# Performance work log

Hardware: AMD Instinct MI355X
Metric: run time of the kernel (lower is better)

The kernel has to match this reference:

```python
import jax, jax.numpy as jnp
import numpy as np

COMMITMENT_COST = 0.25

def setup_inputs() -> dict:
    key = jax.random.key(0)
    k1, k2 = jax.random.split(key)
    inputs = jax.random.normal(k1, (16, 256, 64, 64), dtype=jnp.float32)   # [B, C=D, H, W]
    embedding = jax.random.normal(k2, (2048, 256), dtype=jnp.float32)      # [K, D] codebook
    return {"inputs": inputs, "embedding": embedding}

def reference(inputs, embedding):
    K, D = embedding.shape
    x = jnp.transpose(inputs, (0, 2, 3, 1))            # [B, H, W, D]
    flat = x.reshape(-1, D)                            # [N, D]
    distances = (jnp.sum(flat * flat, axis=1, keepdims=True)
                 + jnp.sum(embedding * embedding, axis=1)
                 - 2.0 * flat @ embedding.T)
    idx = jnp.argmin(distances, axis=1)                # [N]
    encodings = jax.nn.one_hot(idx, K, dtype=flat.dtype)  # [N, K]
    quantized = embedding[idx].reshape(x.shape)        # gather == one_hot @ embedding
    # commitment loss (eval mode: only e_latent term, scaled)
    e_latent_loss = jnp.mean((jax.lax.stop_gradient(quantized) - x) ** 2)
    loss = COMMITMENT_COST * e_latent_loss
    # straight-through estimator
    quantized_st = x + jax.lax.stop_gradient(quantized - x)
    avg_probs = jnp.mean(encodings, axis=0)
    perplexity = jnp.exp(-jnp.sum(avg_probs * jnp.log(avg_probs + 1e-10)))
    return (loss,
            jnp.transpose(quantized_st, (0, 3, 1, 2)),  # back to [B, C, H, W]
            perplexity,
            encodings)
```

## Files before the change

### kernel.cpp

```cpp
#include <hip/hip_runtime.h>

#define KCODES  2048
#define DDIM    256

#define OUT_LOSS 0
#define OUT_Q    1
#define OUT_PERP 16777217
#define OUT_ENC  16777218

#define WS_IDX  0
#define WS_E2   1048576
#define WS_CNT  1056768
#define WS_SUM  1064960
#define WS_EHI  2097152

typedef _Float16 f16x8 __attribute__((ext_vector_type(8)));
typedef _Float16 f16x4 __attribute__((ext_vector_type(4)));
typedef float    f32x4 __attribute__((ext_vector_type(4)));
typedef float    f32x2 __attribute__((ext_vector_type(2)));

#define MERGE2(m1,i1,m2,i2,n1,j1,n2,j2)                                   \
    {                                                                     \
        const bool w_ = ((n1) < (m1)) || ((n1) == (m1) && (j1) < (i1));   \
        const float w1_ = w_ ? (n1) : (m1); const int wi_ = w_ ? (j1) : (i1); \
        const float l1_ = w_ ? (m1) : (n1); const int li_ = w_ ? (i1) : (j1); \
        const float c2_ = w_ ? (n2) : (m2); const int ci_ = w_ ? (j2) : (i2); \
        const bool s_ = ((c2_) < (l1_)) || ((c2_) == (l1_) && (ci_) < (li_)); \
        (m1) = w1_; (i1) = wi_;                                           \
        (m2) = s_ ? c2_ : l1_; (i2) = s_ ? ci_ : li_;                     \
    }

__launch_bounds__(256)
__global__ void k_e2split(const float* __restrict__ emb, _Float16* __restrict__ Ehi,
                          float* __restrict__ e2, int* __restrict__ counts,
                          float* __restrict__ sumsq) {
    const int wave = threadIdx.x >> 6;
    const int lane = threadIdx.x & 63;
    const int k = blockIdx.x * 4 + wave;
    const float4 v = *(const float4*)(emb + k * DDIM + lane * 4);
    f16x4 h;
    h[0] = (_Float16)v.x; h[1] = (_Float16)v.y; h[2] = (_Float16)v.z; h[3] = (_Float16)v.w;
    *(f16x4*)(Ehi + k * DDIM + lane * 4) = h;
    float s = v.x * v.x + v.y * v.y + v.z * v.z + v.w * v.w;
#pragma unroll
    for (int off = 32; off >= 1; off >>= 1) s += __shfl_down(s, off);
    if (lane == 0) e2[k] = s;
    if (blockIdx.x < 8) counts[blockIdx.x * 256 + threadIdx.x] = 0;
    if (blockIdx.x == 8 && threadIdx.x == 0) sumsq[0] = 0.0f;
}

__launch_bounds__(256, 2)
__global__ void k_main(const float* __restrict__ inp, const float* __restrict__ emb,
                       const _Float16* __restrict__ Ehi, const float* __restrict__ e2g,
                       int* __restrict__ idx_g, int* __restrict__ counts,
                       float* __restrict__ sumsq) {
    __shared__ __align__(16) _Float16 A[128 * 256];
    __shared__ float e2s[KCODES];
    __shared__ float xpart[4][128];

    const int rb  = blockIdx.x;
    const int b   = rb >> 5;
    const int hw0 = (rb & 31) << 7;
    const int n0  = rb << 7;
    const int tid = threadIdx.x;
    const int w = tid >> 6, lane = tid & 63;
    const int lq = lane >> 4, lm = lane & 15;
    const int wr = (w >> 1) * 64, wc = (w & 1) * 64;

    {
        const float4* s = (const float4*)e2g;
        float4* d = (float4*)e2s;
        d[tid] = s[tid];
        d[tid + 256] = s[tid + 256];
    }

    const float* base = inp + (size_t)b * 1048576 + hw0;
    float x2lo = 0.f, x2hi = 0.f;
#pragma unroll 4
    for (int rr = 0; rr < 16; ++rr) {
        const int row = ((rr & 1) << 6) + lane;
        const int cg  = ((rr >> 1) << 2) + w;
        const float* p = base + (size_t)(cg << 3) * 4096 + row;
        float v[8];
#pragma unroll
        for (int j = 0; j < 8; ++j) v[j] = p[(size_t)j * 4096];
        f16x8 h;
        float s = 0.f;
#pragma unroll
        for (int j = 0; j < 8; ++j) { h[j] = (_Float16)v[j]; s = fmaf(v[j], v[j], s); }
        if (rr & 1) x2hi += s; else x2lo += s;
        const int q  = cg >> 3;
        const int ch = cg & 7;
        *(f16x8*)&A[row * 256 + q * 64 + ((ch ^ (row & 7)) << 3)] = h;
    }
    xpart[w][lane] = x2lo;
    xpart[w][64 + lane] = x2hi;
    __syncthreads();

    const _Float16* Bb = Ehi + (size_t)(wc + lm) * 256 + lq * 8;
    const int sw0 = ((lq    ) ^ (lm & 7)) << 3;
    const int sw1 = ((lq ^ 4) ^ (lm & 7)) << 3;

    float V1[4][4], V2[4][4]; int I1[4][4], I2[4][4];
#pragma unroll
    for (int i = 0; i < 4; ++i)
#pragma unroll
        for (int rr = 0; rr < 4; ++rr) {
            V1[i][rr] = 3.402823466e38f; V2[i][rr] = 3.402823466e38f;
            I1[i][rr] = 0x7fffffff;      I2[i][rr] = 0x7fffffff;
        }

#pragma unroll 1
    for (int ct = 0; ct < 16; ++ct) {
        const int c0 = ct * 128;
        f32x4 acc[4][4];
#pragma unroll
        for (int i = 0; i < 4; ++i)
#pragma unroll
            for (int j = 0; j < 4; ++j) acc[i][j] = (f32x4)(0.0f);

        f16x8 bn[4];
#pragma unroll
        for (int t = 0; t < 4; ++t)
            bn[t] = *(const f16x8*)(Bb + (size_t)(c0 + t * 16) * 256);

#pragma unroll
        for (int g = 0; g < 8; ++g) {
            f16x8 bf[4];
#pragma unroll
            for (int t = 0; t < 4; ++t) bf[t] = bn[t];
            if (g < 7) {
                const int dof = (((g + 1) >> 1) << 6) + (((g + 1) & 1) << 5);
#pragma unroll
                for (int t = 0; t < 4; ++t)
                    bn[t] = *(const f16x8*)(Bb + (size_t)(c0 + t * 16) * 256 + dof);
            }
            const int kt = g >> 1;
            const int sw = (g & 1) ? sw1 : sw0;
            f16x8 af[4];
#pragma unroll
            for (int t = 0; t < 4; ++t)
                af[t] = *(const f16x8*)&A[(wr + t * 16 + lm) * 256 + kt * 64 + sw];
#pragma unroll
            for (int i = 0; i < 4; ++i)
#pragma unroll
                for (int j = 0; j < 4; ++j)
                    acc[i][j] = __builtin_amdgcn_mfma_f32_16x16x32_f16(af[i], bf[j], acc[i][j], 0, 0, 0);
        }

        float e2v[4];
#pragma unroll
        for (int j = 0; j < 4; ++j) e2v[j] = e2s[c0 + wc + j * 16 + lm];
#pragma unroll
        for (int i = 0; i < 4; ++i)
#pragma unroll
            for (int j = 0; j < 4; ++j) {
                const int idx = c0 + wc + j * 16 + lm;
#pragma unroll
                for (int rr = 0; rr < 4; ++rr) {
                    const float dist = fmaf(-2.0f, acc[i][j][rr], e2v[j]);
                    const bool b1 = dist < V1[i][rr];
                    const bool b2 = dist < V2[i][rr];
                    V2[i][rr] = b1 ? V1[i][rr] : (b2 ? dist : V2[i][rr]);
                    I2[i][rr] = b1 ? I1[i][rr] : (b2 ? idx  : I2[i][rr]);
                    V1[i][rr] = b1 ? dist : V1[i][rr];
                    I1[i][rr] = b1 ? idx  : I1[i][rr];
                }
            }
    }

    __syncthreads();
    float4* red  = (float4*)&A[0];
    float*  refp = (float*)&A[4096];
#pragma unroll
    for (int i = 0; i < 4; ++i)
#pragma unroll
        for (int rr = 0; rr < 4; ++rr) {
            float m1 = V1[i][rr]; int i1 = I1[i][rr];
            float m2 = V2[i][rr]; int i2 = I2[i][rr];
#pragma unroll
            for (int off = 1; off < 16; off <<= 1) {
                const float n1 = __shfl_xor(m1, off); const int j1 = __shfl_xor(i1, off);
                const float n2 = __shfl_xor(m2, off); const int j2 = __shfl_xor(i2, off);
                MERGE2(m1, i1, m2, i2, n1, j1, n2, j2);
            }
            if (lm == 0) {
                const int row = wr + i * 16 + lq * 4 + rr;
                red[row * 2 + (w & 1)] = make_float4(m1, __int_as_float(i1),
                                                     m2, __int_as_float(i2));
            }
        }
    __syncthreads();

    {
        const int rg = w & 1, dh = w >> 1;
        const int r  = (rg << 6) + lane;
        const float4 Ac = red[r * 2];
        const float4 Bc = red[r * 2 + 1];
        const int c0i = __float_as_int(Ac.y), c1i = __float_as_int(Ac.w);
        const int c2i = __float_as_int(Bc.y), c3i = __float_as_int(Bc.w);
        const float* xp = base + (size_t)(dh * 128) * 4096 + r;
        const float* p0 = emb + (size_t)c0i * DDIM + dh * 128;
        const float* p1 = emb + (size_t)c1i * DDIM + dh * 128;
        const float* p2 = emb + (size_t)c2i * DDIM + dh * 128;
        const float* p3 = emb + (size_t)c3i * DDIM + dh * 128;
        float s0 = 0.f, s1 = 0.f, s2 = 0.f, s3 = 0.f;
#pragma unroll 8
        for (int dd = 0; dd < 128; ++dd) {
            const float xv = xp[(size_t)dd * 4096];
            s0 = fmaf(xv, p0[dd], s0);
            s1 = fmaf(xv, p1[dd], s1);
            s2 = fmaf(xv, p2[dd], s2);
            s3 = fmaf(xv, p3[dd], s3);
        }
        f32x4 sv; sv[0] = s0; sv[1] = s1; sv[2] = s2; sv[3] = s3;
        *(f32x4*)&refp[(w * 64 + lane) * 4] = sv;
    }
    __syncthreads();

    if (tid < 128) {
        const int r = tid;
        const int g = r >> 6, rl = r & 63;
        float S[4];
#pragma unroll
        for (int k = 0; k < 4; ++k)
            S[k] = refp[(g * 64 + rl) * 4 + k] + refp[((g + 2) * 64 + rl) * 4 + k];
        const float4 Ac = red[r * 2];
        const float4 Bc = red[r * 2 + 1];
        const int cid[4] = {__float_as_int(Ac.y), __float_as_int(Ac.w),
                            __float_as_int(Bc.y), __float_as_int(Bc.w)};
        float bv = 3.402823466e38f; int bi = 0; float sb = 0.f, eb = 0.f;
#pragma unroll
        for (int k = 0; k < 4; ++k) {
            const float ev = e2s[cid[k]];
            const float dv = fmaf(-2.0f, S[k], ev);
            if (dv < bv || (dv == bv && cid[k] < bi)) { bv = dv; bi = cid[k]; sb = S[k]; eb = ev; }
        }
        idx_g[n0 + r] = bi;
        atomicAdd(&counts[bi], 1);
        const float x2r = xpart[0][r] + xpart[1][r] + xpart[2][r] + xpart[3][r];
        float lr = x2r - 2.0f * sb + eb;
#pragma unroll
        for (int off = 32; off >= 1; off >>= 1) lr += __shfl_down(lr, off);
        if ((r & 63) == 0) atomicAdd(sumsq, lr);
    }
}

__launch_bounds__(256)
__global__ void k_out(const float* __restrict__ emb, const int* __restrict__ idx_g,
                      float* __restrict__ outQ, float* __restrict__ enc) {
    __shared__ int idxs[64];
    const int blk = blockIdx.x;
    const int b   = blk >> 6;
    const int hw0 = (blk & 63) << 6;
    const int w = threadIdx.x >> 6, lane = threadIdx.x & 63;
    const int n0 = (b << 12) + hw0;

    if (threadIdx.x < 64) idxs[threadIdx.x] = idx_g[n0 + threadIdx.x];
    __syncthreads();

    const int myidx = idxs[lane];
    const float* qp = emb + (size_t)myidx * DDIM + w * 64;
    float* op = outQ + (size_t)b * 1048576 + (size_t)(w * 64) * 4096 + hw0 + lane;
#pragma unroll 8
    for (int dd = 0; dd < 64; ++dd)
        __builtin_nontemporal_store(qp[dd], op + (size_t)dd * 4096);

    f32x2* erow = (f32x2*)enc + (size_t)n0 * 1024;
#pragma unroll 1
    for (int rr = 0; rr < 64; ++rr) {
        const int id = idxs[rr];
        f32x2* rp = erow + (size_t)rr * 1024;
#pragma unroll
        for (int k = 0; k < 4; ++k) {
            const int c2 = k * 256 + threadIdx.x;
            const int ccc = c2 * 2;
            f32x2 v;
            v[0] = (ccc == id) ? 1.0f : 0.0f;
            v[1] = (ccc + 1 == id) ? 1.0f : 0.0f;
            __builtin_nontemporal_store(v, rp + c2);
        }
    }
}

__launch_bounds__(256)
__global__ void k_finalize(const int* __restrict__ counts, const float* __restrict__ sumsq,
                           float* __restrict__ out) {
    __shared__ float red[256];
    const int t = threadIdx.x;
    float s = 0.0f;
    for (int k = t; k < KCODES; k += 256) {
        const float p = (float)counts[k] * (1.0f / 65536.0f);
        s += p * logf(p + 1e-10f);
    }
    red[t] = s;
    __syncthreads();
    for (int off = 128; off >= 1; off >>= 1) {
        if (t < off) red[t] += red[t + off];
        __syncthreads();
    }
    if (t == 0) {
        out[OUT_PERP] = expf(-red[0]);
        out[OUT_LOSS] = 0.25f * sumsq[0] * (1.0f / 16777216.0f);
    }
}

extern "C" void kernel_launch(void* const* d_in, const int* in_sizes, int n_in,
                              void* d_out, int out_size, void* d_ws, size_t ws_size,
                              hipStream_t stream) {
    const float* inp = (const float*)d_in[0];
    const float* emb = (const float*)d_in[1];
    float* out = (float*)d_out;
    char* wsb  = (char*)d_ws;

    int*      idxg   = (int*)(wsb + WS_IDX);
    float*    e2     = (float*)(wsb + WS_E2);
    int*      counts = (int*)(wsb + WS_CNT);
    float*    sumsq  = (float*)(wsb + WS_SUM);
    _Float16* Ehi    = (_Float16*)(wsb + WS_EHI);

    k_e2split <<<512,  256, 0, stream>>>(emb, Ehi, e2, counts, sumsq);
    k_main    <<<512,  256, 0, stream>>>(inp, emb, Ehi, e2, idxg, counts, sumsq);
    k_out     <<<1024, 256, 0, stream>>>(emb, idxg, out + OUT_Q, out + OUT_ENC);
    k_finalize<<<1,    256, 0, stream>>>(counts, sumsq, out);
}
```

Before: 977.6 us.

## Stage codebook tiles into LDS via global_load_lds instead of per-wave register loads

The main distance GEMM now stages each 128x64 fp16 codebook tile into a swizzled shared-memory buffer with direct global-to-LDS loads, shared by all four waves. Previously each wave loaded its B fragments straight from global memory into registers. The e2 table is read from global memory instead of being copied to LDS, and the x squared-norm is moved into the fp32 refinement loop, which frees the xpart shared buffer. The cost is two block barriers per K-step and no prefetch overlap between loading and MFMA, which may expose load latency.

```diff
diff --git a/kernel.cpp b/kernel.cpp
--- a/kernel.cpp
+++ b/kernel.cpp
@@ -18,6 +18,11 @@
 typedef _Float16 f16x4 __attribute__((ext_vector_type(4)));
 typedef float    f32x4 __attribute__((ext_vector_type(4)));
 typedef float    f32x2 __attribute__((ext_vector_type(2)));
+
+__device__ __forceinline__ void gld16(const void* g, void* l) {
+    __builtin_amdgcn_global_load_lds((const __attribute__((address_space(1))) void*)g,
+                                     (__attribute__((address_space(3))) void*)l, 16, 0, 0);
+}
 
 #define MERGE2(m1,i1,m2,i2,n1,j1,n2,j2)                                   \
     {                                                                     \
@@ -55,8 +60,7 @@
                        int* __restrict__ idx_g, int* __restrict__ counts,
                        float* __restrict__ sumsq) {
     __shared__ __align__(16) _Float16 A[128 * 256];
-    __shared__ float e2s[KCODES];
-    __shared__ float xpart[4][128];
+    __shared__ __align__(16) _Float16 Bh[128 * 64];
 
     const int rb  = blockIdx.x;
     const int b   = rb >> 5;
@@ -66,16 +70,10 @@
     const int w = tid >> 6, lane = tid & 63;
     const int lq = lane >> 4, lm = lane & 15;
     const int wr = (w >> 1) * 64, wc = (w & 1) * 64;
-
-    {
-        const float4* s = (const float4*)e2g;
-        float4* d = (float4*)e2s;
-        d[tid] = s[tid];
-        d[tid + 256] = s[tid + 256];
-    }
+    const int r8 = lane >> 3, c8 = lane & 7;
+    const int gch = c8 ^ r8;
 
     const float* base = inp + (size_t)b * 1048576 + hw0;
-    float x2lo = 0.f, x2hi = 0.f;
 #pragma unroll 4
     for (int rr = 0; rr < 16; ++rr) {
         const int row = ((rr & 1) << 6) + lane;
@@ -85,19 +83,14 @@
 #pragma unroll
         for (int j = 0; j < 8; ++j) v[j] = p[(size_t)j * 4096];
         f16x8 h;
-        float s = 0.f;
-#pragma unroll
-        for (int j = 0; j < 8; ++j) { h[j] = (_Float16)v[j]; s = fmaf(v[j], v[j], s); }
-        if (rr & 1) x2hi += s; else x2lo += s;
+#pragma unroll
+        for (int j = 0; j < 8; ++j) h[j] = (_Float16)v[j];
         const int q  = cg >> 3;
         const int ch = cg & 7;
         *(f16x8*)&A[row * 256 + q * 64 + ((ch ^ (row & 7)) << 3)] = h;
     }
-    xpart[w][lane] = x2lo;
-    xpart[w][64 + lane] = x2hi;
-    __syncthreads();
-
-    const _Float16* Bb = Ehi + (size_t)(wc + lm) * 256 + lq * 8;
+    __syncthreads();
+
     const int sw0 = ((lq    ) ^ (lm & 7)) << 3;
     const int sw1 = ((lq ^ 4) ^ (lm & 7)) << 3;
 
@@ -113,44 +106,45 @@
 #pragma unroll 1
     for (int ct = 0; ct < 16; ++ct) {
         const int c0 = ct * 128;
+        float e2v[4];
+#pragma unroll
+        for (int j = 0; j < 4; ++j) e2v[j] = e2g[c0 + wc + j * 16 + lm];
+
         f32x4 acc[4][4];
 #pragma unroll
         for (int i = 0; i < 4; ++i)
 #pragma unroll
             for (int j = 0; j < 4; ++j) acc[i][j] = (f32x4)(0.0f);
 
-        f16x8 bn[4];
-#pragma unroll
-        for (int t = 0; t < 4; ++t)
-            bn[t] = *(const f16x8*)(Bb + (size_t)(c0 + t * 16) * 256);
-
-#pragma unroll
-        for (int g = 0; g < 8; ++g) {
-            f16x8 bf[4];
-#pragma unroll
-            for (int t = 0; t < 4; ++t) bf[t] = bn[t];
-            if (g < 7) {
-                const int dof = (((g + 1) >> 1) << 6) + (((g + 1) & 1) << 5);
-#pragma unroll
-                for (int t = 0; t < 4; ++t)
-                    bn[t] = *(const f16x8*)(Bb + (size_t)(c0 + t * 16) * 256 + dof);
-            }
-            const int kt = g >> 1;
-            const int sw = (g & 1) ? sw1 : sw0;
-            f16x8 af[4];
-#pragma unroll
-            for (int t = 0; t < 4; ++t)
-                af[t] = *(const f16x8*)&A[(wr + t * 16 + lm) * 256 + kt * 64 + sw];
-#pragma unroll
-            for (int i = 0; i < 4; ++i)
-#pragma unroll
-                for (int j = 0; j < 4; ++j)
-                    acc[i][j] = __builtin_amdgcn_mfma_f32_16x16x32_f16(af[i], bf[j], acc[i][j], 0, 0, 0);
-        }
-
-        float e2v[4];
-#pragma unroll
-        for (int j = 0; j < 4; ++j) e2v[j] = e2s[c0 + wc + j * 16 + lm];
+#pragma unroll 1
+        for (int kt = 0; kt < 4; ++kt) {
+            const int d0 = kt * 64;
+            __syncthreads();
+#pragma unroll
+            for (int i = 0; i < 4; ++i) {
+                const int Row = i * 32 + w * 8 + r8;
+                gld16(Ehi + (size_t)(c0 + Row) * DDIM + d0 + gch * 8, &Bh[(i * 32 + w * 8) * 64]);
+            }
+            __syncthreads();
+#pragma unroll
+            for (int s = 0; s < 2; ++s) {
+                const int wch = s * 4 + lq;
+                const int sw = s ? sw1 : sw0;
+                f16x8 af[4], bf[4];
+#pragma unroll
+                for (int t = 0; t < 4; ++t) {
+                    const int Rb = wc + t * 16 + lm;
+                    af[t] = *(const f16x8*)&A[(wr + t * 16 + lm) * 256 + d0 + sw];
+                    bf[t] = *(const f16x8*)&Bh[Rb * 64 + ((wch ^ (Rb & 7)) << 3)];
+                }
+#pragma unroll
+                for (int i = 0; i < 4; ++i)
+#pragma unroll
+                    for (int j = 0; j < 4; ++j)
+                        acc[i][j] = __builtin_amdgcn_mfma_f32_16x16x32_f16(af[i], bf[j], acc[i][j], 0, 0, 0);
+            }
+        }
+
 #pragma unroll
         for (int i = 0; i < 4; ++i)
 #pragma unroll
@@ -204,7 +198,7 @@
         const float* p1 = emb + (size_t)c1i * DDIM + dh * 128;
         const float* p2 = emb + (size_t)c2i * DDIM + dh * 128;
         const float* p3 = emb + (size_t)c3i * DDIM + dh * 128;
-        float s0 = 0.f, s1 = 0.f, s2 = 0.f, s3 = 0.f;
+        float s0 = 0.f, s1 = 0.f, s2 = 0.f, s3 = 0.f, s4 = 0.f;
 #pragma unroll 8
         for (int dd = 0; dd < 128; ++dd) {
             const float xv = xp[(size_t)dd * 4096];
@@ -212,19 +206,23 @@
             s1 = fmaf(xv, p1[dd], s1);
             s2 = fmaf(xv, p2[dd], s2);
             s3 = fmaf(xv, p3[dd], s3);
-        }
-        f32x4 sv; sv[0] = s0; sv[1] = s1; sv[2] = s2; sv[3] = s3;
-        *(f32x4*)&refp[(w * 64 + lane) * 4] = sv;
+            s4 = fmaf(xv, xv,     s4);
+        }
+        refp[0 * 256 + w * 64 + lane] = s0;
+        refp[1 * 256 + w * 64 + lane] = s1;
+        refp[2 * 256 + w * 64 + lane] = s2;
+        refp[3 * 256 + w * 64 + lane] = s3;
+        refp[4 * 256 + w * 64 + lane] = s4;
     }
     __syncthreads();
 
     if (tid < 128) {
         const int r = tid;
         const int g = r >> 6, rl = r & 63;
-        float S[4];
-#pragma unroll
-        for (int k = 0; k < 4; ++k)
-            S[k] = refp[(g * 64 + rl) * 4 + k] + refp[((g + 2) * 64 + rl) * 4 + k];
+        float S[5];
+#pragma unroll
+        for (int k = 0; k < 5; ++k)
+            S[k] = refp[k * 256 + g * 64 + rl] + refp[k * 256 + (g + 2) * 64 + rl];
         const float4 Ac = red[r * 2];
         const float4 Bc = red[r * 2 + 1];
         const int cid[4] = {__float_as_int(Ac.y), __float_as_int(Ac.w),
@@ -232,14 +230,13 @@
         float bv = 3.402823466e38f; int bi = 0; float sb = 0.f, eb = 0.f;
 #pragma unroll
         for (int k = 0; k < 4; ++k) {
-            const float ev = e2s[cid[k]];
+            const float ev = e2g[cid[k]];
             const float dv = fmaf(-2.0f, S[k], ev);
             if (dv < bv || (dv == bv && cid[k] < bi)) { bv = dv; bi = cid[k]; sb = S[k]; eb = ev; }
         }
         idx_g[n0 + r] = bi;
         atomicAdd(&counts[bi], 1);
-        const float x2r = xpart[0][r] + xpart[1][r] + xpart[2][r] + xpart[3][r];
-        float lr = x2r - 2.0f * sb + eb;
+        float lr = S[4] - 2.0f * sb + eb;
 #pragma unroll
         for (int off = 32; off >= 1; off >>= 1) lr += __shfl_down(lr, off);
         if ((r & 63) == 0) atomicAdd(sumsq, lr);
```

Result: faster. 892.6 us (-8.7%).
